# Performance work log

Hardware: AMD Instinct MI355X
Metric: run time of the kernel (lower is better)

Reference implementation:

```python
import jax, jax.numpy as jnp
import numpy as np
import math

D_MODEL = 1024
N_HEADS = 16
D_FF = 4096
EPS = 1e-6
NEG = -1e9


def layer_norm(x, gamma, beta):
    # Faithful to torch: std with Bessel correction (ddof=1), eps added to std.
    mean = jnp.mean(x, axis=-1, keepdims=True)
    std = jnp.std(x, axis=-1, keepdims=True, ddof=1)
    return gamma * ((x - mean) / (std + EPS)) + beta


def mha(x_q, x_kv, wq, bq, wk, bk, wv, bv, wo, bo, mask):
    B, Sq, D = x_q.shape
    Sk = x_kv.shape[1]
    dk = D // N_HEADS
    q = (x_q @ wq + bq).reshape(B, Sq, N_HEADS, dk).transpose(0, 2, 1, 3)
    k = (x_kv @ wk + bk).reshape(B, Sk, N_HEADS, dk).transpose(0, 2, 1, 3)
    v = (x_kv @ wv + bv).reshape(B, Sk, N_HEADS, dk).transpose(0, 2, 1, 3)
    scores = jnp.einsum('bhqd,bhkd->bhqk', q, k) / math.sqrt(dk)
    scores = jnp.where(mask == 0, NEG, scores)
    attn = jax.nn.softmax(scores, axis=-1)
    out = jnp.einsum('bhqk,bhkd->bhqd', attn, v)
    out = out.transpose(0, 2, 1, 3).reshape(B, Sq, D)
    return out @ wo + bo


def setup_inputs() -> dict:
    key = jax.random.key(0)
    ks = jax.random.split(key, 24)
    B, S, D = 2, 2048, D_MODEL
    sc = 0.02
    lin = lambda k, i, o: jax.random.normal(k, (i, o), jnp.float32) * sc
    inp = {
        'x': jax.random.normal(ks[0], (B, S, D), jnp.float32),
        'encoder_output': jax.random.normal(ks[1], (B, S, D), jnp.float32),
        'src_mask': jnp.ones((1, 1, 1, S), jnp.int32),
        'tgt_mask': jnp.tril(jnp.ones((S, S), jnp.int32))[None, None],
        # self-attention params
        'sa_wq': lin(ks[2], D, D), 'sa_bq': jnp.zeros((D,), jnp.float32),
        'sa_wk': lin(ks[3], D, D), 'sa_bk': jnp.zeros((D,), jnp.float32),
        'sa_wv': lin(ks[4], D, D), 'sa_bv': jnp.zeros((D,), jnp.float32),
        'sa_wo': lin(ks[5], D, D), 'sa_bo': jnp.zeros((D,), jnp.float32),
        # cross-attention params
        'ca_wq': lin(ks[6], D, D), 'ca_bq': jnp.zeros((D,), jnp.float32),
        'ca_wk': lin(ks[7], D, D), 'ca_bk': jnp.zeros((D,), jnp.float32),
        'ca_wv': lin(ks[8], D, D), 'ca_bv': jnp.zeros((D,), jnp.float32),
        'ca_wo': lin(ks[9], D, D), 'ca_bo': jnp.zeros((D,), jnp.float32),
        # feed-forward params
        'ff_w1': lin(ks[10], D, D_FF), 'ff_b1': jnp.zeros((D_FF,), jnp.float32),
        'ff_w2': lin(ks[11], D_FF, D), 'ff_b2': jnp.zeros((D,), jnp.float32),
        # layer norms (3 residual connections)
        'n1_g': jnp.ones((D,), jnp.float32), 'n1_b': jnp.zeros((D,), jnp.float32),
        'n2_g': jnp.ones((D,), jnp.float32), 'n2_b': jnp.zeros((D,), jnp.float32),
        'n3_g': jnp.ones((D,), jnp.float32), 'n3_b': jnp.zeros((D,), jnp.float32),
    }
    return inp


def reference(x, encoder_output, src_mask, tgt_mask,
              sa_wq, sa_bq, sa_wk, sa_bk, sa_wv, sa_bv, sa_wo, sa_bo,
              ca_wq, ca_bq, ca_wk, ca_bk, ca_wv, ca_bv, ca_wo, ca_bo,
              ff_w1, ff_b1, ff_w2, ff_b2,
              n1_g, n1_b, n2_g, n2_b, n3_g, n3_b):
    # Pre-norm residual block 1: self-attention (dropout=0 -> identity)
    h = layer_norm(x, n1_g, n1_b)
    x = x + mha(h, h, sa_wq, sa_bq, sa_wk, sa_bk, sa_wv, sa_bv, sa_wo, sa_bo, tgt_mask)
    # Block 2: cross-attention over encoder output
    h = layer_norm(x, n2_g, n2_b)
    x = x + mha(h, encoder_output, ca_wq, ca_bq, ca_wk, ca_bk, ca_wv, ca_bv, ca_wo, ca_bo, src_mask)
    # Block 3: feed-forward
    h = layer_norm(x, n3_g, n3_b)
    ff = jax.nn.relu(h @ ff_w1 + ff_b1) @ ff_w2 + ff_b2
    return x + ff
```

## Files before the change

### kernel.cpp

```cpp
#include <hip/hip_runtime.h>

typedef short short8 __attribute__((ext_vector_type(8)));
typedef float f32x4 __attribute__((ext_vector_type(4)));

#define SEQ 2048
#define QSCALE 0.18033688011112042f
#define PSHIFT 20.0f
#define EXP2(x) __builtin_amdgcn_exp2f(x)

#define GLDS(g, l) __builtin_amdgcn_global_load_lds( \
    (const __attribute__((address_space(1))) unsigned int*)(g), \
    (__attribute__((address_space(3))) unsigned int*)(l), 16, 0, 0)

__device__ __forceinline__ unsigned short f2bf(float f) {
    unsigned int u = __builtin_bit_cast(unsigned int, f);
    unsigned int r = (u + 0x7fffu + ((u >> 16) & 1u)) >> 16;
    return (unsigned short)r;
}

__global__ __launch_bounds__(256)
void wtrans8_kernel(const float* w0, const float* w1, const float* w2, const float* w3,
                    const float* w4, const float* w5, const float* w6, const float* w7,
                    unsigned short* __restrict__ outbase)
{
    const float* Ws[8] = {w0, w1, w2, w3, w4, w5, w6, w7};
    const float* __restrict__ W = Ws[blockIdx.z];
    unsigned short* __restrict__ Wt = outbase + (size_t)blockIdx.z * 1024 * 1024;
    __shared__ float t[32][33];
    const int tx = threadIdx.x & 31;
    const int ty = threadIdx.x >> 5;
    const int nb = blockIdx.x * 32;
    const int kb = blockIdx.y * 32;
#pragma unroll
    for (int i = 0; i < 4; i++)
        t[ty + i * 8][tx] = W[(size_t)(kb + ty + i * 8) * 1024 + nb + tx];
    __syncthreads();
#pragma unroll
    for (int i = 0; i < 4; i++)
        Wt[(size_t)(nb + ty + i * 8) * 1024 + kb + tx] = f2bf(t[tx][ty + i * 8]);
}

__global__ __launch_bounds__(256)
void wtrans_kernel(const float* __restrict__ W, unsigned short* __restrict__ Wt,
                   int Kd, int Nd)
{
    __shared__ float t[32][33];
    const int tx = threadIdx.x & 31;
    const int ty = threadIdx.x >> 5;
    const int nb = blockIdx.x * 32;
    const int kb = blockIdx.y * 32;
#pragma unroll
    for (int i = 0; i < 4; i++)
        t[ty + i * 8][tx] = W[(size_t)(kb + ty + i * 8) * Nd + nb + tx];
    __syncthreads();
#pragma unroll
    for (int i = 0; i < 4; i++)
        Wt[(size_t)(nb + ty + i * 8) * Kd + kb + tx] = f2bf(t[tx][ty + i * 8]);
}

__global__ __launch_bounds__(256)
void cvt_kernel(const float* __restrict__ in, unsigned short* __restrict__ out, int n)
{
    int i = (blockIdx.x * 256 + threadIdx.x) * 4;
    if (i < n) {
        float4 v = *(const float4*)(in + i);
        ushort4 o;
        o.x = f2bf(v.x); o.y = f2bf(v.y); o.z = f2bf(v.z); o.w = f2bf(v.w);
        *(ushort4*)(out + i) = o;
    }
}

__global__ __launch_bounds__(256)
void ln_kernel(const float* __restrict__ x, const float* __restrict__ g,
               const float* __restrict__ bb, unsigned short* __restrict__ out)
{
    const int D = 1024;
    const int row = blockIdx.x;
    const float* xr = x + (size_t)row * D;
    float v[4];
    float s = 0.f, ss = 0.f;
#pragma unroll
    for (int i = 0; i < 4; i++) {
        v[i] = xr[threadIdx.x + i * 256];
        s += v[i];
        ss += v[i] * v[i];
    }
#pragma unroll
    for (int off = 1; off < 64; off <<= 1) {
        s  += __shfl_xor(s,  off, 64);
        ss += __shfl_xor(ss, off, 64);
    }
    __shared__ float red[8];
    const int wave = threadIdx.x >> 6;
    if ((threadIdx.x & 63) == 0) { red[wave] = s; red[4 + wave] = ss; }
    __syncthreads();
    s  = red[0] + red[1] + red[2] + red[3];
    ss = red[4] + red[5] + red[6] + red[7];
    float mean = s / D;
    float var  = fmaxf((ss - s * mean) / (D - 1), 0.f);
    float inv  = 1.f / (sqrtf(var) + 1e-6f);
#pragma unroll
    for (int i = 0; i < 4; i++) {
        int c = threadIdx.x + i * 256;
        out[(size_t)row * D + c] = f2bf(g[c] * (v[i] - mean) * inv + bb[c]);
    }
}

template <int MODE>
__global__ __launch_bounds__(256)
void gemm_kernel(const unsigned short* __restrict__ A,
                 const unsigned short* __restrict__ A2,
                 const unsigned short* __restrict__ Wt,
                 const float* __restrict__ b0,
                 const float* __restrict__ b1,
                 const float* __restrict__ b2,
                 unsigned short* __restrict__ o0,
                 unsigned short* __restrict__ o1,
                 unsigned short* __restrict__ o2,
                 int M, int N, int K)
{
    __shared__ unsigned short As[128 * 32];
    __shared__ unsigned short Bs[128 * 32];
    const int tid  = threadIdx.x;
    const int lane = tid & 63;
    const int wv   = tid >> 6;
    const int quad = lane >> 4;
    const int l16  = lane & 15;
    const int m0 = blockIdx.y * 128;
    const int n0 = blockIdx.x * 128;
    const int wm = (wv >> 1) << 6;
    const int wn = (wv & 1) << 6;
    const int sect = (MODE == 1) ? (n0 >> 10) : 0;
    const unsigned short* Asel = (MODE == 1 && sect != 0) ? A2 : A;

    const int srow0 = wv * 32 + (lane >> 2);
    const int srow1 = srow0 + 16;
    const int scol8 = (lane & 3) * 8;
    unsigned short* asw0 = &As[(wv * 2 + 0) * 512];
    unsigned short* asw1 = &As[(wv * 2 + 1) * 512];
    unsigned short* bsw0 = &Bs[(wv * 2 + 0) * 512];
    unsigned short* bsw1 = &Bs[(wv * 2 + 1) * 512];
    const unsigned short* Ag0 = Asel + (size_t)(m0 + srow0) * K + scol8;
    const unsigned short* Ag1 = Asel + (size_t)(m0 + srow1) * K + scol8;
    const unsigned short* Bg0 = Wt   + (size_t)(n0 + srow0) * K + scol8;
    const unsigned short* Bg1 = Wt   + (size_t)(n0 + srow1) * K + scol8;

    f32x4 acc[4][4];
#pragma unroll
    for (int i = 0; i < 4; i++)
#pragma unroll
        for (int j = 0; j < 4; j++) acc[i][j] = f32x4{0.f, 0.f, 0.f, 0.f};

    for (int k0 = 0; k0 < K; k0 += 32) {
        GLDS(Ag0 + k0, asw0);
        GLDS(Ag1 + k0, asw1);
        GLDS(Bg0 + k0, bsw0);
        GLDS(Bg1 + k0, bsw1);
        __syncthreads();
        short8 af[4], bfr[4];
#pragma unroll
        for (int i = 0; i < 4; i++)
            af[i] = *(const short8*)(&As[(wm + i * 16 + l16) * 32 + quad * 8]);
#pragma unroll
        for (int i = 0; i < 4; i++)
            bfr[i] = *(const short8*)(&Bs[(wn + i * 16 + l16) * 32 + quad * 8]);
#pragma unroll
        for (int mi = 0; mi < 4; mi++)
#pragma unroll
            for (int ni = 0; ni < 4; ni++)
                acc[mi][ni] = __builtin_amdgcn_mfma_f32_16x16x32_bf16(
                    af[mi], bfr[ni], acc[mi][ni], 0, 0, 0);
        __syncthreads();
    }

    if (MODE == 1) {
        const float* bias = (sect == 0) ? b0 : ((sect == 1) ? b1 : b2);
        if (sect == 2) {
#pragma unroll
            for (int mi = 0; mi < 4; mi++)
#pragma unroll
                for (int ni = 0; ni < 4; ni++) {
                    const int cc = (n0 + wn + ni * 16 + l16) & 1023;
                    const int h = cc >> 6, d = cc & 63;
                    const float bv = bias[cc];
                    const int rowg = m0 + wm + mi * 16 + quad * 4;
                    const int b = rowg >> 11, s = rowg & 2047;
                    ushort4 o4;
                    o4.x = f2bf(acc[mi][ni][0] + bv);
                    o4.y = f2bf(acc[mi][ni][1] + bv);
                    o4.z = f2bf(acc[mi][ni][2] + bv);
                    o4.w = f2bf(acc[mi][ni][3] + bv);
                    *(ushort4*)&o2[((size_t)(b * 16 + h) * 64 + d) * SEQ + s] = o4;
                }
        } else {
            unsigned short* dst = (sect == 0) ? o0 : o1;
            const float scl = (sect == 0) ? QSCALE : 1.0f;
#pragma unroll
            for (int mi = 0; mi < 4; mi++)
#pragma unroll
                for (int ni = 0; ni < 4; ni++) {
                    const int cc = (n0 + wn + ni * 16 + l16) & 1023;
                    const int h = cc >> 6, d = cc & 63;
                    const float bv = bias[cc];
#pragma unroll
                    for (int r = 0; r < 4; r++) {
                        const int rowg = m0 + wm + mi * 16 + quad * 4 + r;
                        const int b = rowg >> 11, s = rowg & 2047;
                        float v = (acc[mi][ni][r] + bv) * scl;
                        dst[((size_t)(b * 16 + h) * SEQ + s) * 64 + d] = f2bf(v);
                    }
                }
        }
    } else {
#pragma unroll
        for (int mi = 0; mi < 4; mi++)
#pragma unroll
            for (int ni = 0; ni < 4; ni++) {
                const int colg = n0 + wn + ni * 16 + l16;
                const float bv = b0[colg];
#pragma unroll
                for (int r = 0; r < 4; r++) {
                    const int rowg = m0 + wm + mi * 16 + quad * 4 + r;
                    float v = acc[mi][ni][r] + bv;
                    o0[(size_t)rowg * N + colg] = f2bf(fmaxf(v, 0.f));
                }
            }
    }
}

__global__ __launch_bounds__(256, 1)
void gemm_db_kernel(const unsigned short* __restrict__ A,
                    const unsigned short* __restrict__ Wt,
                    const float* __restrict__ b0,
                    const float* __restrict__ res,
                    float* __restrict__ outf,
                    int M, int N, int K, int cm, int cn)
{
    __shared__ unsigned short As[3][128 * 64];
    __shared__ unsigned short Bs[3][128 * 64];
    const int tid  = threadIdx.x;
    const int lane = tid & 63;
    const int wv   = tid >> 6;
    const int quad = lane >> 4;
    const int l16  = lane & 15;
    const int NX  = gridDim.x;
    const int id  = blockIdx.y * NX + blockIdx.x;
    const int xcd = id & 7, slot = id >> 3;
    const int ngx = NX / cn;
    const int rg = xcd / ngx, cg = xcd - rg * ngx;
    const int m0 = (rg * cm + (slot % cm)) * 128;
    const int n0 = (cg * cn + (slot / cm)) * 128;
    const int wm = (wv >> 1) << 6;
    const int wn = (wv & 1) << 6;

    const int rsub = lane >> 3;
    const int cu8  = ((lane & 7) ^ rsub) * 8;
    const unsigned short* Ag = A  + (size_t)(m0 + wv * 32 + rsub) * K + cu8;
    const unsigned short* Bg = Wt + (size_t)(n0 + wv * 32 + rsub) * K + cu8;

    f32x4 acc[4][4];
#pragma unroll
    for (int i = 0; i < 4; i++)
#pragma unroll
        for (int j = 0; j < 4; j++) acc[i][j] = f32x4{0.f, 0.f, 0.f, 0.f};

    const int NT = K >> 6;

    auto stage = [&](int t, int b) {
        const int kb = t << 6;
#pragma unroll
        for (int r = 0; r < 4; r++) {
            GLDS(Ag + (size_t)(r * 8) * K + kb, &As[b][(wv * 4 + r) * 512]);
            GLDS(Bg + (size_t)(r * 8) * K + kb, &Bs[b][(wv * 4 + r) * 512]);
        }
    };

    stage(0, 0);
    if (NT > 1) stage(1, 1);

    for (int i = 0; i < NT; i++) {
        const int b = i % 3;
        if (i + 2 < NT) {
            stage(i + 2, (i + 2) % 3);
            asm volatile("s_waitcnt vmcnt(16)" ::: "memory");
        } else if (i + 1 < NT) {
            asm volatile("s_waitcnt vmcnt(8)" ::: "memory");
        } else {
            asm volatile("s_waitcnt vmcnt(0)" ::: "memory");
        }
        __builtin_amdgcn_s_barrier();

#pragma unroll
        for (int ks = 0; ks < 2; ks++) {
            short8 af[4], bfr[4];
#pragma unroll
            for (int mi = 0; mi < 4; mi++)
                af[mi] = *(const short8*)(&As[b][(wm + mi * 16 + l16) * 64 +
                             (((ks * 4 + quad) ^ (l16 & 7)) * 8)]);
#pragma unroll
            for (int ni = 0; ni < 4; ni++)
                bfr[ni] = *(const short8*)(&Bs[b][(wn + ni * 16 + l16) * 64 +
                             (((ks * 4 + quad) ^ (l16 & 7)) * 8)]);
#pragma unroll
            for (int mi = 0; mi < 4; mi++)
#pragma unroll
                for (int ni = 0; ni < 4; ni++)
                    acc[mi][ni] = __builtin_amdgcn_mfma_f32_16x16x32_bf16(
                        af[mi], bfr[ni], acc[mi][ni], 0, 0, 0);
        }
        asm volatile("s_waitcnt lgkmcnt(0)" ::: "memory");
        __builtin_amdgcn_s_barrier();
    }

#pragma unroll
    for (int mi = 0; mi < 4; mi++)
#pragma unroll
        for (int ni = 0; ni < 4; ni++) {
            const int colg = n0 + wn + ni * 16 + l16;
            const float bv = b0[colg];
#pragma unroll
            for (int r = 0; r < 4; r++) {
                const int rowg = m0 + wm + mi * 16 + quad * 4 + r;
                outf[(size_t)rowg * N + colg] =
                    acc[mi][ni][r] + bv + res[(size_t)rowg * N + colg];
            }
        }
}

template <bool CAUSAL>
__global__ __launch_bounds__(256, 2)
void attn4_kernel(const unsigned short* __restrict__ Q,
                  const unsigned short* __restrict__ K,
                  const unsigned short* __restrict__ VT,
                  unsigned short* __restrict__ O)
{
    __shared__ unsigned short Ks[128 * 72];
    __shared__ unsigned short Vt[64 * 136];
    __shared__ unsigned short Ps[4][32 * 136];
    __shared__ float sumS[4][32];
    const int tid  = threadIdx.x;
    const int lane = tid & 63;
    const int wave = tid >> 6;
    const int quad = lane >> 4;
    const int l16  = lane & 15;
    const int bh = blockIdx.y;
    const int qb = (CAUSAL && (bh & 16)) ? (15 - (int)blockIdx.x) : (int)blockIdx.x;
    const int q0 = qb * 128;
    const size_t baseK = (size_t)bh * SEQ * 64;
    const size_t baseV = (size_t)bh * 64 * SEQ;

    short8 aq[2][2];
#pragma unroll
    for (int qs = 0; qs < 2; qs++) {
        const unsigned short* qp =
            Q + baseK + (size_t)(q0 + wave * 32 + qs * 16 + l16) * 64 + quad * 8;
        aq[qs][0] = *(const short8*)(qp);
        aq[qs][1] = *(const short8*)(qp + 32);
    }
    f32x4 acc[4][2];
#pragma unroll
    for (int i = 0; i < 4; i++)
#pragma unroll
        for (int j = 0; j < 2; j++) acc[i][j] = f32x4{0.f, 0.f, 0.f, 0.f};
    float lsum[2][4] = {{0.f, 0.f, 0.f, 0.f}, {0.f, 0.f, 0.f, 0.f}};

    const int nkb = CAUSAL ? (qb + 1) : (SEQ / 128);
    const int krow = tid >> 1;
    const int kc   = (tid & 1) * 32;
    const int vrow = tid >> 2;
    const int vc   = (tid & 3) * 32;
    const unsigned short* kg = K  + baseK + (size_t)krow * 64 + kc;
    const unsigned short* vg = VT + baseV + (size_t)vrow * SEQ + vc;

    short8 kr0 = *(const short8*)(kg),      kr1 = *(const short8*)(kg + 8);
    short8 kr2 = *(const short8*)(kg + 16), kr3 = *(const short8*)(kg + 24);
    short8 vr0 = *(const short8*)(vg),      vr1 = *(const short8*)(vg + 8);
    short8 vr2 = *(const short8*)(vg + 16), vr3 = *(const short8*)(vg + 24);

    for (int kb = 0; kb < nkb; kb++) {
        __syncthreads();
        *(short8*)&Ks[krow * 72 + kc]      = kr0;
        *(short8*)&Ks[krow * 72 + kc + 8]  = kr1;
        *(short8*)&Ks[krow * 72 + kc + 16] = kr2;
        *(short8*)&Ks[krow * 72 + kc + 24] = kr3;
        *(short8*)&Vt[vrow * 136 + vc]      = vr0;
        *(short8*)&Vt[vrow * 136 + vc + 8]  = vr1;
        *(short8*)&Vt[vrow * 136 + vc + 16] = vr2;
        *(short8*)&Vt[vrow * 136 + vc + 24] = vr3;
        if (kb + 1 < nkb) {
            const unsigned short* kg2 = kg + (size_t)(kb + 1) * 128 * 64;
            const unsigned short* vg2 = vg + (size_t)(kb + 1) * 128;
            kr0 = *(const short8*)(kg2);      kr1 = *(const short8*)(kg2 + 8);
            kr2 = *(const short8*)(kg2 + 16); kr3 = *(const short8*)(kg2 + 24);
            vr0 = *(const short8*)(vg2);      vr1 = *(const short8*)(vg2 + 8);
            vr2 = *(const short8*)(vg2 + 16); vr3 = *(const short8*)(vg2 + 24);
        }
        __syncthreads();

        const bool maskTile = CAUSAL && (kb == nkb - 1);
#pragma unroll
        for (int qs = 0; qs < 2; qs++) {
            f32x4 scf[8];
#pragma unroll
            for (int nt = 0; nt < 8; nt++) {
                f32x4 z = f32x4{0.f, 0.f, 0.f, 0.f};
#pragma unroll
                for (int c = 0; c < 2; c++) {
                    short8 bk = *(const short8*)(&Ks[(nt * 16 + l16) * 72 + c * 32 + quad * 8]);
                    z = __builtin_amdgcn_mfma_f32_16x16x32_bf16(aq[qs][c], bk, z, 0, 0, 0);
                }
                scf[nt] = z;
            }
            if (maskTile) {
                const int qg = q0 + wave * 32 + qs * 16 + quad * 4;
                const int k0 = kb * 128;
#pragma unroll
                for (int nt = 0; nt < 8; nt++) {
                    const int kg_ = k0 + nt * 16 + l16;
#pragma unroll
                    for (int r = 0; r < 4; r++)
                        if (kg_ > qg + r) scf[nt][r] = -1e9f;
                }
            }
#pragma unroll
            for (int nt = 0; nt < 8; nt++)
#pragma unroll
                for (int r = 0; r < 4; r++) {
                    float pv = EXP2(scf[nt][r] - PSHIFT);
                    lsum[qs][r] += pv;
                    Ps[wave][(qs * 16 + quad * 4 + r) * 136 +
                             ((nt * 16 + l16) ^ (quad * 8))] = f2bf(pv);
                }
        }
        const int pswz = 8 * (quad ^ ((l16 >> 2) & 3));
#pragma unroll
        for (int c = 0; c < 4; c++) {
            short8 av[4];
#pragma unroll
            for (int mi = 0; mi < 4; mi++)
                av[mi] = *(const short8*)(&Vt[(mi * 16 + l16) * 136 + c * 32 + quad * 8]);
#pragma unroll
            for (int qs = 0; qs < 2; qs++) {
                short8 bp = *(const short8*)(&Ps[wave][(qs * 16 + l16) * 136 + c * 32 + pswz]);
#pragma unroll
                for (int mi = 0; mi < 4; mi++)
                    acc[mi][qs] = __builtin_amdgcn_mfma_f32_16x16x32_bf16(av[mi], bp, acc[mi][qs], 0, 0, 0);
            }
        }
    }
#pragma unroll
    for (int qs = 0; qs < 2; qs++)
#pragma unroll
        for (int r = 0; r < 4; r++) {
#pragma unroll
            for (int off = 1; off < 16; off <<= 1)
                lsum[qs][r] += __shfl_xor(lsum[qs][r], off, 64);
        }
    if (l16 == 0) {
#pragma unroll
        for (int qs = 0; qs < 2; qs++)
#pragma unroll
            for (int r = 0; r < 4; r++)
                sumS[wave][qs * 16 + quad * 4 + r] = lsum[qs][r];
    }
    __syncthreads();
    const int b = bh >> 4, h = bh & 15;
#pragma unroll
    for (int qs = 0; qs < 2; qs++) {
        const float rcpL = 1.f / sumS[wave][qs * 16 + l16];
        const int qg = q0 + wave * 32 + qs * 16 + l16;
#pragma unroll
        for (int mi = 0; mi < 4; mi++) {
            ushort4 o4;
            o4.x = f2bf(acc[mi][qs][0] * rcpL);
            o4.y = f2bf(acc[mi][qs][1] * rcpL);
            o4.z = f2bf(acc[mi][qs][2] * rcpL);
            o4.w = f2bf(acc[mi][qs][3] * rcpL);
            *(ushort4*)&O[(size_t)(b * SEQ + qg) * 1024 + h * 64 + mi * 16 + quad * 4] = o4;
        }
    }
}

extern "C" void kernel_launch(void* const* d_in, const int* in_sizes, int n_in,
                              void* d_out, int out_size, void* d_ws, size_t ws_size,
                              hipStream_t stream)
{
    (void)in_sizes; (void)n_in; (void)out_size; (void)ws_size;
    const int B = 2, S = SEQ, D = 1024, DFF = 4096;
    const int M = B * S;

    const float* x     = (const float*)d_in[0];
    const float* enc   = (const float*)d_in[1];
    const float* sa_wq = (const float*)d_in[4],  *sa_bq = (const float*)d_in[5];
    const float* sa_wk = (const float*)d_in[6],  *sa_bk = (const float*)d_in[7];
    const float* sa_wv = (const float*)d_in[8],  *sa_bv = (const float*)d_in[9];
    const float* sa_wo = (const float*)d_in[10], *sa_bo = (const float*)d_in[11];
    const float* ca_wq = (const float*)d_in[12], *ca_bq = (const float*)d_in[13];
    const float* ca_wk = (const float*)d_in[14], *ca_bk = (const float*)d_in[15];
    const float* ca_wv = (const float*)d_in[16], *ca_bv = (const float*)d_in[17];
    const float* ca_wo = (const float*)d_in[18], *ca_bo = (const float*)d_in[19];
    const float* ff_w1 = (const float*)d_in[20], *ff_b1 = (const float*)d_in[21];
    const float* ff_w2 = (const float*)d_in[22], *ff_b2 = (const float*)d_in[23];
    const float* n1_g  = (const float*)d_in[24], *n1_b = (const float*)d_in[25];
    const float* n2_g  = (const float*)d_in[26], *n2_b = (const float*)d_in[27];
    const float* n3_g  = (const float*)d_in[28], *n3_b = (const float*)d_in[29];
    float* out = (float*)d_out;

    char* p = (char*)d_ws;
    auto carve = [&](size_t bytes) -> char* {
        char* r = p;
        p += (bytes + 255) & ~(size_t)255;
        return r;
    };
    unsigned short* wt8     = (unsigned short*)carve((size_t)8 * D * D * 2);
    unsigned short* wt_sqkv = wt8;
    unsigned short* wt_sao  = wt8 + (size_t)3 * D * D;
    unsigned short* wt_cqkv = wt8 + (size_t)4 * D * D;
    unsigned short* wt_cao  = wt8 + (size_t)7 * D * D;
    unsigned short* wt_ff1  = (unsigned short*)carve((size_t)D * DFF * 2);
    unsigned short* wt_ff2  = (unsigned short*)carve((size_t)DFF * D * 2);
    unsigned short* encb    = (unsigned short*)carve((size_t)M * D * 2);
    unsigned short* hb      = (unsigned short*)carve((size_t)M * D * 2);
    unsigned short* qbuf    = (unsigned short*)carve((size_t)M * D * 2);
    unsigned short* kbuf    = (unsigned short*)carve((size_t)M * D * 2);
    unsigned short* vtbuf   = (unsigned short*)carve((size_t)M * D * 2);
    unsigned short* ffh     = (unsigned short*)carve((size_t)M * DFF * 2);
    float* x1 = (float*)carve((size_t)M * D * 4);
    unsigned short* abuf = hb;
    float* x2 = out;

    dim3 blk(256);
    wtrans8_kernel<<<dim3(32, 32, 8), blk, 0, stream>>>(
        sa_wq, sa_wk, sa_wv, sa_wo, ca_wq, ca_wk, ca_wv, ca_wo, wt8);
    wtrans_kernel<<<dim3(DFF / 32, D / 32), blk, 0, stream>>>(ff_w1, wt_ff1, D, DFF);
    wtrans_kernel<<<dim3(D / 32, DFF / 32), blk, 0, stream>>>(ff_w2, wt_ff2, DFF, D);
    cvt_kernel<<<dim3(M * D / 1024), blk, 0, stream>>>(enc, encb, M * D);

    ln_kernel<<<dim3(M), blk, 0, stream>>>(x, n1_g, n1_b, hb);
    gemm_kernel<1><<<dim3(3 * D / 128, M / 128), blk, 0, stream>>>(
        hb, hb, wt_sqkv, sa_bq, sa_bk, sa_bv, qbuf, kbuf, vtbuf, M, 3 * D, D);
    attn4_kernel<true><<<dim3(S / 128, B * 16), blk, 0, stream>>>(qbuf, kbuf, vtbuf, abuf);
    gemm_db_kernel<<<dim3(D / 128, M / 128), blk, 0, stream>>>(
        abuf, wt_sao, sa_bo, x, x1, M, D, D, 8, 4);

    ln_kernel<<<dim3(M), blk, 0, stream>>>(x1, n2_g, n2_b, hb);
    gemm_kernel<1><<<dim3(3 * D / 128, M / 128), blk, 0, stream>>>(
        hb, encb, wt_cqkv, ca_bq, ca_bk, ca_bv, qbuf, kbuf, vtbuf, M, 3 * D, D);
    attn4_kernel<false><<<dim3(S / 128, B * 16), blk, 0, stream>>>(qbuf, kbuf, vtbuf, abuf);
    gemm_db_kernel<<<dim3(D / 128, M / 128), blk, 0, stream>>>(
        abuf, wt_cao, ca_bo, x1, x2, M, D, D, 8, 4);

    ln_kernel<<<dim3(M), blk, 0, stream>>>(x2, n3_g, n3_b, hb);
    gemm_kernel<2><<<dim3(DFF / 128, M / 128), blk, 0, stream>>>(
        hb, hb, wt_ff1, ff_b1, nullptr, nullptr, ffh, nullptr, nullptr, M, DFF, D);
    gemm_db_kernel<<<dim3(D / 128, M / 128), blk, 0, stream>>>(
        ffh, wt_ff2, ff_b2, x2, out, M, D, DFF, 4, 8);
}
```

Measured before the change: 594.3 us.

## Replace direct global-to-LDS triple buffering with register-staged double buffering in residual GEMM

The residual GEMM kernel previously used global_load_lds to stream tiles straight into a three-deep LDS ring. It now loads the next tile into registers while computing on the current one, then writes those registers into the other half of a two-deep LDS buffer. This cuts LDS use and the vmcnt bookkeeping, but adds register pressure and extra LDS write instructions. The prefetch distance also drops from two tiles to one, so global latency is hidden less well.

After: 582.2 us. -2.0%, faster.

```diff
diff --git a/kernel.cpp b/kernel.cpp
--- a/kernel.cpp
+++ b/kernel.cpp
@@ -236,8 +236,8 @@
                     float* __restrict__ outf,
                     int M, int N, int K, int cm, int cn)
 {
-    __shared__ unsigned short As[3][128 * 64];
-    __shared__ unsigned short Bs[3][128 * 64];
+    __shared__ unsigned short As[2][128 * 64];
+    __shared__ unsigned short Bs[2][128 * 64];
     const int tid  = threadIdx.x;
     const int lane = tid & 63;
     const int wv   = tid >> 6;
@@ -266,40 +266,44 @@
 
     const int NT = K >> 6;
 
-    auto stage = [&](int t, int b) {
+    short8 ar[4], br[4];
+
+    auto ldregs = [&](int t) {
         const int kb = t << 6;
 #pragma unroll
         for (int r = 0; r < 4; r++) {
-            GLDS(Ag + (size_t)(r * 8) * K + kb, &As[b][(wv * 4 + r) * 512]);
-            GLDS(Bg + (size_t)(r * 8) * K + kb, &Bs[b][(wv * 4 + r) * 512]);
+            ar[r] = *(const short8*)(Ag + (size_t)(r * 8) * K + kb);
+            br[r] = *(const short8*)(Bg + (size_t)(r * 8) * K + kb);
         }
     };
-
-    stage(0, 0);
-    if (NT > 1) stage(1, 1);
+    auto wrlds = [&](int b) {
+#pragma unroll
+        for (int r = 0; r < 4; r++) {
+            *(short8*)&As[b][(wv * 4 + r) * 512 + lane * 8] = ar[r];
+            *(short8*)&Bs[b][(wv * 4 + r) * 512 + lane * 8] = br[r];
+        }
+    };
+
+    ldregs(0);
+    asm volatile("s_waitcnt vmcnt(0)" ::: "memory");
+    wrlds(0);
+    asm volatile("s_waitcnt lgkmcnt(0)" ::: "memory");
+    __builtin_amdgcn_s_barrier();
 
     for (int i = 0; i < NT; i++) {
-        const int b = i % 3;
-        if (i + 2 < NT) {
-            stage(i + 2, (i + 2) % 3);
-            asm volatile("s_waitcnt vmcnt(16)" ::: "memory");
-        } else if (i + 1 < NT) {
-            asm volatile("s_waitcnt vmcnt(8)" ::: "memory");
-        } else {
-            asm volatile("s_waitcnt vmcnt(0)" ::: "memory");
-        }
-        __builtin_amdgcn_s_barrier();
+        const int cur = i & 1;
+        if (i + 1 < NT) ldregs(i + 1);
 
 #pragma unroll
         for (int ks = 0; ks < 2; ks++) {
             short8 af[4], bfr[4];
 #pragma unroll
             for (int mi = 0; mi < 4; mi++)
-                af[mi] = *(const short8*)(&As[b][(wm + mi * 16 + l16) * 64 +
+                af[mi] = *(const short8*)(&As[cur][(wm + mi * 16 + l16) * 64 +
                              (((ks * 4 + quad) ^ (l16 & 7)) * 8)]);
 #pragma unroll
             for (int ni = 0; ni < 4; ni++)
-                bfr[ni] = *(const short8*)(&Bs[b][(wn + ni * 16 + l16) * 64 +
+                bfr[ni] = *(const short8*)(&Bs[cur][(wn + ni * 16 + l16) * 64 +
                              (((ks * 4 + quad) ^ (l16 & 7)) * 8)]);
 #pragma unroll
             for (int mi = 0; mi < 4; mi++)
@@ -308,8 +312,13 @@
                     acc[mi][ni] = __builtin_amdgcn_mfma_f32_16x16x32_bf16(
                         af[mi], bfr[ni], acc[mi][ni], 0, 0, 0);
         }
-        asm volatile("s_waitcnt lgkmcnt(0)" ::: "memory");
-        __builtin_amdgcn_s_barrier();
+
+        if (i + 1 < NT) {
+            asm volatile("s_waitcnt vmcnt(0)" ::: "memory");
+            wrlds(cur ^ 1);
+            asm volatile("s_waitcnt lgkmcnt(0)" ::: "memory");
+            __builtin_amdgcn_s_barrier();
+        }
     }
 
 #pragma unroll
```
